# Optimization experiments

Hardware: AMD Instinct MI355X
Metric: run time of the kernel (lower is better)

## Reference

```python
import jax, jax.numpy as jnp
from jax import lax
import numpy as np

B, T = 128, 28
N = T - 1  # 27 recurrent steps


def conv(x, w, b, stride=1, pad=1):
    y = lax.conv_general_dilated(x, w, (stride, stride), [(pad, pad), (pad, pad)],
                                 dimension_numbers=('NCHW', 'OIHW', 'NCHW'))
    return y + b[None, :, None, None]


def convT(x, w, b, stride, pad, out_pad):
    # torch ConvTranspose2d: weight layout [in, out, k, k]
    k = w.shape[-1]
    wt = jnp.flip(w, (-2, -1)).transpose(1, 0, 2, 3)  # -> [out, in, k, k]
    lo, hi = k - 1 - pad, k - 1 - pad + out_pad
    y = lax.conv_general_dilated(x, wt, (1, 1), [(lo, hi), (lo, hi)],
                                 lhs_dilation=(stride, stride),
                                 dimension_numbers=('NCHW', 'OIHW', 'NCHW'))
    return y + b[None, :, None, None]


def setup_inputs():
    key = jax.random.key(0)
    ki = iter(jax.random.split(key, 48))
    def cw(o, i, k=3):
        return jax.random.normal(next(ki), (o, i, k, k), jnp.float32) / np.sqrt(i * k * k)
    def bias(o):
        return jax.random.normal(next(ki), (o,), jnp.float32) * 0.02
    H, I = 16 * 8 * 8, 48 * 8 * 8
    return {
        'x': jax.random.uniform(next(ki), (B, T, 3, 32, 32), jnp.float32),
        'eps': jax.random.normal(next(ki), (N, B, 64, 8, 8), jnp.float32),
        'psix1_w': cw(16, 3),  'psix1_b': bias(16),
        'psix2_w': cw(16, 16), 'psix2_b': bias(16),
        'psiz_w': cw(16, 64),  'psiz_b': bias(16),
        'enc1_w': cw(32, 32),  'enc1_b': bias(32),
        'enc2_w': cw(64, 32),  'enc2_b': bias(64),
        'encm_w': cw(64, 64),  'encm_b': bias(64),
        'encv_w': cw(64, 64),  'encv_b': bias(64),
        'pri_w': cw(32, 16),   'pri_b': bias(32),
        'prim_w': cw(64, 32),  'prim_b': bias(64),
        'priv_w': cw(64, 32),  'priv_b': bias(64),
        'dec1_w': jax.random.normal(next(ki), (32, 32, 3, 3), jnp.float32) / np.sqrt(32 * 9),
        'dec1_b': bias(32),
        'dec2_w': jax.random.normal(next(ki), (32, 3, 3, 3), jnp.float32) / np.sqrt(32 * 9),
        'dec2_b': bias(3),
        'gru_wi': jax.random.normal(next(ki), (3 * H, I), jnp.float32) / np.sqrt(I),
        'gru_wh': jax.random.normal(next(ki), (3 * H, H), jnp.float32) / np.sqrt(H),
        'gru_bi': bias(3 * H),
        'gru_bh': bias(3 * H),
    }


def _forward(x, eps, psix1_w, psix1_b, psix2_w, psix2_b, psiz_w, psiz_b,
             enc1_w, enc1_b, enc2_w, enc2_b, encm_w, encm_b, encv_w, encv_b,
             pri_w, pri_b, prim_w, prim_b, priv_w, priv_b,
             dec1_w, dec1_b, dec2_w, dec2_b, gru_wi, gru_wh, gru_bi, gru_bh):
    Bn = x.shape[0]
    Hf = 16 * 8 * 8
    n = x.shape[1] - 1

    def step(carry, inputs):
        h0, dec_prev, _, _, _, _ = carry
        frame, ep, idx = inputs
        cur = jnp.where(idx < 6, frame, dec_prev)
        px = jax.nn.relu(conv(cur, psix1_w, psix1_b, 2, 1))   # [B,16,16,16]
        px = jax.nn.relu(conv(px, psix2_w, psix2_b, 2, 1))    # [B,16,8,8]
        e = jnp.concatenate([px, h0], axis=1)                 # [B,32,8,8]
        e = jax.nn.relu(conv(e, enc1_w, enc1_b))
        e = jax.nn.relu(conv(e, enc2_w, enc2_b))              # [B,64,8,8]
        zm = conv(e, encm_w, encm_b)
        zlv = jax.nn.softplus(conv(e, encv_w, encv_b))
        p = jax.nn.relu(conv(h0, pri_w, pri_b))               # [B,32,8,8]
        pm = conv(p, prim_w, prim_b)
        plv = jax.nn.softplus(conv(p, priv_w, priv_b))
        z = zm + zlv * ep                                     # source's literal reparam (uses logvar, not std)
        zpsi = jax.nn.relu(conv(z, psiz_w, psiz_b))           # [B,16,8,8]
        d = jnp.concatenate([h0, zpsi], axis=1)               # [B,32,8,8]
        d = jax.nn.relu(convT(d, dec1_w, dec1_b, 2, 1, 0))    # 8 -> 15
        dec = jax.nn.sigmoid(convT(d, dec2_w, dec2_b, 2, 0, 1))  # 15 -> 32, [B,3,32,32]
        # GRUCell on flattened concat
        gi = jnp.concatenate([px, zpsi, h0], axis=1).reshape(Bn, -1)  # [B, 48*8*8]
        hf = h0.reshape(Bn, Hf)
        gih = gi @ gru_wi.T + gru_bi
        ghh = hf @ gru_wh.T + gru_bh
        ir, iz, inn = jnp.split(gih, 3, axis=1)
        hr, hz, hn = jnp.split(ghh, 3, axis=1)
        r = jax.nn.sigmoid(ir + hr)
        u = jax.nn.sigmoid(iz + hz)
        ng = jnp.tanh(inn + r * hn)
        hnew = ((1.0 - u) * ng + u * hf).reshape(Bn, 16, 8, 8)
        return (hnew, dec, zm, zlv, pm, plv), dec

    h0 = jnp.zeros((Bn, 16, 8, 8), jnp.float32)
    dec0 = jnp.zeros((Bn, 3, 32, 32), jnp.float32)
    s0 = jnp.zeros((Bn, 64, 8, 8), jnp.float32)
    frames = jnp.swapaxes(x[:, :n], 0, 1)  # [N,B,3,32,32]
    (_, _, zm, zlv, pm, plv), decs = lax.scan(
        step, (h0, dec0, s0, s0, s0, s0), (frames, eps, jnp.arange(n)))
    output = jnp.swapaxes(decs, 0, 1)  # [B,N,3,32,32]
    return output, zm, zlv, pm, plv


def reference(x, eps, psix1_w, psix1_b, psix2_w, psix2_b, psiz_w, psiz_b,
              enc1_w, enc1_b, enc2_w, enc2_b, encm_w, encm_b, encv_w, encv_b,
              pri_w, pri_b, prim_w, prim_b, priv_w, priv_b,
              dec1_w, dec1_b, dec2_w, dec2_b, gru_wi, gru_wh, gru_bi, gru_bh):
    return _forward(x, eps, psix1_w, psix1_b, psix2_w, psix2_b, psiz_w, psiz_b,
                    enc1_w, enc1_b, enc2_w, enc2_b, encm_w, encm_b, encv_w, encv_b,
                    pri_w, pri_b, prim_w, prim_b, priv_w, priv_b,
                    dec1_w, dec1_b, dec2_w, dec2_b, gru_wi, gru_wh, gru_bi, gru_bh)
```

## Files before the change

### kernel.cpp

```cpp
#include <hip/hip_runtime.h>

#define NSTEP 27

typedef _Float16 f16;
typedef __attribute__((ext_vector_type(8))) _Float16 f16x8;
typedef __attribute__((ext_vector_type(4))) float f32x4;

#define MFMA(a, b, c) __builtin_amdgcn_mfma_f32_16x16x32_f16(a, b, c, 0, 0, 0)

__device__ __forceinline__ float sigmoidf_(float x) { return 1.0f / (1.0f + expf(-x)); }
__device__ __forceinline__ float softplusf_(float x) { return x > 20.0f ? x : log1pf(expf(x)); }

constexpr long OFF_WI   = 0;
constexpr long OFF_WH   = OFF_WI   + 3072L * 3072;
constexpr long OFF_WPX1 = OFF_WH   + 3072L * 1024;
constexpr long OFF_WPX2 = OFF_WPX1 + 512;
constexpr long OFF_WE1  = OFF_WPX2 + 2560;
constexpr long OFF_WE2  = OFF_WE1  + 9216;
constexpr long OFF_WMV  = OFF_WE2  + 18432;
constexpr long OFF_WPZ  = OFF_WMV  + 73728;
constexpr long OFF_WPRI = OFF_WPZ  + 9216;
constexpr long OFF_WPMV = OFF_WPRI + 5120;
constexpr long OFF_WD1  = OFF_WPMV + 36864;
constexpr long OFF_GI   = OFF_WD1  + 9216;
constexpr long OFF_F16_END = OFF_GI + 128L * 3072;

struct Params {
  const float* frame; long fstride;
  const float* eps_t;
  const f16 *wpx1, *wpx2, *we1, *we2, *wmv, *wpz, *wd1, *wpri, *wpmv;
  const float *bpx1, *bpx2, *be1, *be2, *bm, *bv, *bpz, *bd1;
  const float *d2w, *d2b, *bpri, *bpm, *bpv, *gbi, *gbh;
  const float *gih0, *gih1, *ghh;
  float* hG; f16* gi;
  float *out_t, *zm, *zlv, *pm, *plv;
  int t, last;
};

__device__ __forceinline__ void scat8_lds(f16* __restrict__ A, int ldk, int pos, int ic, float val) {
  int py = pos >> 3, px = pos & 7;
  f16 v = (f16)val;
#pragma unroll
  for (int ky = 0; ky < 3; ++ky) {
    int oy = py + 1 - ky;
    if ((unsigned)oy >= 8u) continue;
#pragma unroll
    for (int kx = 0; kx < 3; ++kx) {
      int ox = px + 1 - kx;
      if ((unsigned)ox >= 8u) continue;
      A[(oy * 8 + ox) * ldk + ic * 9 + ky * 3 + kx] = v;
    }
  }
}

__device__ __forceinline__ void scatd1_lds(f16* __restrict__ Ad1, int pos, int ic, float val) {
  const int aof[4] = {0, 2560, 7168, 11776};
  const int Kp[4] = {40, 72, 72, 136};
  int py = pos >> 3, px = pos & 7;
  f16 v = (f16)val;
#pragma unroll
  for (int ky = 0; ky < 3; ++ky) {
    int y = 2 * py + ky - 1;
    if ((unsigned)y >= 15u) continue;
    int cy = y & 1;
    int nky = cy ? 2 : 1;
    int tiy = cy ? (ky >> 1) : 0;
#pragma unroll
    for (int kx = 0; kx < 3; ++kx) {
      int x = 2 * px + kx - 1;
      if ((unsigned)x >= 15u) continue;
      int cx = x & 1;
      int nkx = cx ? 2 : 1;
      int tix = cx ? (kx >> 1) : 0;
      int c = cy * 2 + cx;
      Ad1[aof[c] + ((y >> 1) * 8 + (x >> 1)) * Kp[c] + ic * (nky * nkx) + tiy * nkx + tix] = v;
    }
  }
}

__global__ __launch_bounds__(256) void k_wpack(const float* __restrict__ src, f16* __restrict__ dst,
                                               int N, int Ks, int Kd) {
  int tot = N * Kd, stride = gridDim.x * 256;
  for (int i = blockIdx.x * 256 + threadIdx.x; i < tot; i += stride) {
    int n = i / Kd, k = i - n * Kd;
    dst[i] = (k < Ks) ? (f16)src[n * Ks + k] : (f16)0.f;
  }
}

__global__ __launch_bounds__(256) void k_wd1(const float* __restrict__ src, f16* __restrict__ dst) {
  int i = blockIdx.x * 256 + threadIdx.x;
  if (i >= 9216) return;
  int c, base;
  if (i < 1024) { c = 0; base = 0; }
  else if (i < 3072) { c = 1; base = 1024; }
  else if (i < 5120) { c = 2; base = 3072; }
  else { c = 3; base = 5120; }
  const int Kc[4] = {32, 64, 64, 128};
  int j = i - base, K = Kc[c];
  int oc = j / K, k = j - oc * K;
  int cy = c >> 1, cx = c & 1;
  int nky = cy ? 2 : 1, nkx = cx ? 2 : 1, ntap = nky * nkx;
  int ic = k / ntap, tap = k - ic * ntap;
  int tiy = tap / nkx, tix = tap - tiy * nkx;
  int ky = (nky == 1) ? 1 : tiy * 2;
  int kx = (nkx == 1) ? 1 : tix * 2;
  dst[i] = (f16)src[((ic * 32 + oc) * 3 + ky) * 3 + kx];
}

__global__ __launch_bounds__(1024) void k_step(Params P) {
  __shared__ f16 lds[78336];
  f16* hbuf = lds;
  f16* B1 = lds + 1024;
  f16* B2 = lds + 38400;
  f16* B3 = lds + 57344;
  f16* A1 = B3;
  f16* frame = B3 + 10240;
  f16* A2 = B3 + 10240;

  int b = blockIdx.x, tid = threadIdx.x;
  int wv = tid >> 6, lane = tid & 63, lm = lane & 15, q = lane >> 4;
  f32x4 z4 = {};

  {
    int i = tid;
    float hn = 0.f;
    if (P.t) {
      long o = (long)b * 3072 + i;
      float ir  = P.gih0[o] + P.gih1[o] + P.gbi[i];
      float iz  = P.gih0[o + 1024] + P.gih1[o + 1024] + P.gbi[i + 1024];
      float in_ = P.gih0[o + 2048] + P.gih1[o + 2048] + P.gbi[i + 2048];
      float hr  = P.ghh[o] + P.gbh[i];
      float hz  = P.ghh[o + 1024] + P.gbh[i + 1024];
      float hnn = P.ghh[o + 2048] + P.gbh[i + 2048];
      float r = sigmoidf_(ir + hr), u = sigmoidf_(iz + hz);
      float ng = tanhf(in_ + r * hnn);
      hn = (1.f - u) * ng + u * P.hG[b * 1024 + i];
    }
    P.hG[b * 1024 + i] = hn;
    hbuf[i] = (f16)hn;
    P.gi[(long)b * 3072 + 2048 + i] = (f16)hn;
  }
  const float* fr = P.frame + (long)b * P.fstride;
  for (int i = tid; i < 3072; i += 1024) frame[i] = (f16)fr[i];
  __syncthreads();
  if (tid < 512) {
    int row = tid >> 1, half = tid & 1;
    int oy = row >> 4, ox = row & 15;
    f16* rp = A1 + row * 40;
    if (half == 0) {
#pragma unroll
      for (int ic = 0; ic < 2; ++ic)
#pragma unroll
        for (int ky = 0; ky < 3; ++ky) {
          int y = 2 * oy + ky - 1;
#pragma unroll
          for (int kx = 0; kx < 3; ++kx) {
            int x = 2 * ox + kx - 1;
            rp[ic * 9 + ky * 3 + kx] =
                ((unsigned)y < 32u && (unsigned)x < 32u) ? frame[ic * 1024 + y * 32 + x] : (f16)0;
          }
        }
    } else {
#pragma unroll
      for (int ky = 0; ky < 3; ++ky) {
        int y = 2 * oy + ky - 1;
#pragma unroll
        for (int kx = 0; kx < 3; ++kx) {
          int x = 2 * ox + kx - 1;
          rp[18 + ky * 3 + kx] =
              ((unsigned)y < 32u && (unsigned)x < 32u) ? frame[2048 + y * 32 + x] : (f16)0;
        }
      }
#pragma unroll
      for (int k = 27; k < 40; ++k) rp[k] = (f16)0;
    }
  } else {
    int4 zz = {0, 0, 0, 0};
    int t2 = tid - 512;
    for (int i = t2; i < 18944 / 8; i += 512) ((int4*)B2)[i] = zz;
    for (int i = t2; i < 37376 / 8; i += 512) ((int4*)B1)[i] = zz;
  }
  __syncthreads();
  {
    int4 zz = {0, 0, 0, 0};
    for (int i = tid; i < 10752 / 8; i += 1024) ((int4*)A2)[i] = zz;
  }
  __syncthreads();
  scat8_lds(B2, 296, tid & 63, 16 + (tid >> 6), (float)hbuf[tid]);
  {
    f16x8 bf = *(const f16x8*)(P.wpx1 + lm * 32 + q * 8);
    float bb = P.bpx1[lm];
    int mt = wv;
    f16x8 a = *(const f16x8*)(A1 + (mt * 16 + lm) * 40 + q * 8);
    f32x4 acc = MFMA(a, bf, z4);
#pragma unroll
    for (int r = 0; r < 4; ++r) {
      int m = mt * 16 + q * 4 + r;
      float val = fmaxf(acc[r] + bb, 0.f);
      int y = m >> 4, x = m & 15;
      f16 v = (f16)val;
#pragma unroll
      for (int ky = 0; ky < 3; ++ky) {
        int ty = y + 1 - ky;
        if (ty < 0 || (ty & 1)) continue;
        int oy = ty >> 1; if (oy >= 8) continue;
#pragma unroll
        for (int kx = 0; kx < 3; ++kx) {
          int tx = x + 1 - kx;
          if (tx < 0 || (tx & 1)) continue;
          int ox = tx >> 1; if (ox >= 8) continue;
          A2[(oy * 8 + ox) * 168 + lm * 9 + ky * 3 + kx] = v;
        }
      }
    }
  }
  __syncthreads();
  if (wv < 4) {
    f32x4 acc = {};
#pragma unroll
    for (int k = 0; k < 160; k += 32) {
      f16x8 a = *(const f16x8*)(A2 + (wv * 16 + lm) * 168 + k + q * 8);
      f16x8 bf = *(const f16x8*)(P.wpx2 + lm * 160 + k + q * 8);
      acc = MFMA(a, bf, acc);
    }
    float bb = P.bpx2[lm];
#pragma unroll
    for (int r = 0; r < 4; ++r) {
      int pos = wv * 16 + q * 4 + r;
      float val = fmaxf(acc[r] + bb, 0.f);
      P.gi[(long)b * 3072 + lm * 64 + pos] = (f16)val;
      scat8_lds(B2, 296, pos, lm, val);
    }
  }
  __syncthreads();
  {
    int nt = wv & 1, mt = (wv >> 1) & 3;
    f32x4 a0 = {};
    if (wv < 8) {
#pragma unroll
      for (int k = 0; k < 288; k += 32) {
        f16x8 bf = *(const f16x8*)(P.we1 + (nt * 16 + lm) * 288 + k + q * 8);
        f16x8 x0 = *(const f16x8*)(B2 + (mt * 16 + lm) * 296 + k + q * 8);
        a0 = MFMA(x0, bf, a0);
      }
    } else {
      int i0 = (wv - 8) * 128 + lane;
      scatd1_lds(B3, i0 & 63, i0 >> 6, (float)hbuf[i0]);
      int i1 = i0 + 64;
      scatd1_lds(B3, i1 & 63, i1 >> 6, (float)hbuf[i1]);
    }
    __syncthreads();
    if (wv < 8) {
      float bb = P.be1[nt * 16 + lm];
#pragma unroll
      for (int r = 0; r < 4; ++r)
        scat8_lds(B2, 296, mt * 16 + q * 4 + r, nt * 16 + lm, fmaxf(a0[r] + bb, 0.f));
    }
  }
  __syncthreads();
  {
    int nt = wv & 3, mh = wv >> 2;
    f32x4 acc = {};
#pragma unroll
    for (int k = 0; k < 288; k += 32) {
      f16x8 bf = *(const f16x8*)(P.we2 + (nt * 16 + lm) * 288 + k + q * 8);
      f16x8 a = *(const f16x8*)(B2 + ((mh)*16 + lm) * 296 + k + q * 8);
      acc = MFMA(a, bf, acc);
    }
    int ch = nt * 16 + lm;
    float bb = P.be2[ch];
#pragma unroll
    for (int r = 0; r < 4; ++r)
      scat8_lds(B1, 584, mh * 16 + q * 4 + r, ch, fmaxf(acc[r] + bb, 0.f));
  }
  __syncthreads();
  {
    f32x4 am = {}, av = {};
    int nq = wv & 3, mh = wv >> 2;
    int ch = nq * 16 + lm;
#pragma unroll
    for (int k = 0; k < 576; k += 32) {
      f16x8 bm = *(const f16x8*)(P.wmv + (long)ch * 576 + k + q * 8);
      f16x8 bv = *(const f16x8*)(P.wmv + (long)(64 + ch) * 576 + k + q * 8);
      f16x8 a = *(const f16x8*)(B1 + (mh * 16 + lm) * 584 + k + q * 8);
      am = MFMA(a, bm, am);
      av = MFMA(a, bv, av);
    }
    __syncthreads();
    float bbm = P.bm[ch], bbv = P.bv[ch];
#pragma unroll
    for (int r = 0; r < 4; ++r) {
      int pos = mh * 16 + q * 4 + r;
      float zmv = am[r] + bbm;
      float sp = softplusf_(av[r] + bbv);
      float zval = zmv + sp * P.eps_t[(long)b * 4096 + ch * 64 + pos];
      if (P.last) {
        P.zm[(long)b * 4096 + ch * 64 + pos] = zmv;
        P.zlv[(long)b * 4096 + ch * 64 + pos] = sp;
      }
      scat8_lds(B1, 584, pos, ch, zval);
    }
  }
  __syncthreads();
  if (wv < 4) {
    f32x4 acc = {};
#pragma unroll
    for (int k = 0; k < 576; k += 32) {
      f16x8 a = *(const f16x8*)(B1 + (wv * 16 + lm) * 584 + k + q * 8);
      f16x8 bf = *(const f16x8*)(P.wpz + (long)lm * 576 + k + q * 8);
      acc = MFMA(a, bf, acc);
    }
    float bb = P.bpz[lm];
#pragma unroll
    for (int r = 0; r < 4; ++r) {
      int pos = wv * 16 + q * 4 + r;
      float val = fmaxf(acc[r] + bb, 0.f);
      P.gi[(long)b * 3072 + 1024 + lm * 64 + pos] = (f16)val;
      scatd1_lds(B3, pos, 16 + lm, val);
    }
  }
  __syncthreads();
  {
    int nt = wv & 1, mt = (wv >> 1) & 3, cb = wv >> 3;
#pragma unroll
    for (int cc = 0; cc < 2; ++cc) {
      int c = cb + cc * 2;
      int cy = c >> 1, cx = c & 1;
      int Kc = 32 << (cy + cx);
      int Kp = Kc + 8;
      int aof = cy ? (cx ? 11776 : 7168) : (cx ? 2560 : 0);
      int bof = cy ? (cx ? 5120 : 3072) : (cx ? 1024 : 0);
      f32x4 acc = {};
      for (int k = 0; k < Kc; k += 32) {
        f16x8 a = *(const f16x8*)(B3 + aof + (mt * 16 + lm) * Kp + k + q * 8);
        f16x8 bf = *(const f16x8*)(P.wd1 + bof + (nt * 16 + lm) * Kc + k + q * 8);
        acc = MFMA(a, bf, acc);
      }
      int oc = nt * 16 + lm;
      float bb = P.bd1[oc];
#pragma unroll
      for (int r = 0; r < 4; ++r) {
        int m = mt * 16 + q * 4 + r;
        int y = 2 * (m >> 3) + cy, x = 2 * (m & 7) + cx;
        if (y < 15 && x < 15)
          B2[oc * 240 + y * 15 + x] = (f16)fmaxf(acc[r] + bb, 0.f);
      }
    }
  }
  __syncthreads();
  {
    int p = wv & 3, jh = wv >> 2;
    int cy2 = p >> 1, cx2 = p & 1;
    int lx = lane & 15, ly = lane >> 4;
    int x = 2 * lx + cx2;
    float acc0 = P.d2b[0], acc1 = P.d2b[1], acc2 = P.d2b[2];
    int nky = cy2 ? 1 : 2, nkx = cx2 ? 1 : 2;
    int py = jh * 4 + ly;
    for (int ic = 0; ic < 32; ++ic) {
      const f16* sp = B2 + ic * 240;
      const float* wic = P.d2w + ic * 27;
      for (int ty = 0; ty < nky; ++ty) {
        int ky = cy2 ? 1 : ty * 2;
        int iy = (2 * py + cy2 - ky) >> 1;
        bool yv = (unsigned)iy < 15u;
        for (int tx = 0; tx < nkx; ++tx) {
          int kx = cx2 ? 1 : tx * 2;
          int ix = (x - kx) >> 1;
          if (yv && (unsigned)ix < 15u) {
            float v = (float)sp[iy * 15 + ix];
            acc0 += v * wic[ky * 3 + kx];
            acc1 += v * wic[9 + ky * 3 + kx];
            acc2 += v * wic[18 + ky * 3 + kx];
          }
        }
      }
    }
    int y = 2 * py + cy2;
    P.out_t[(long)b * 82944 + 0 * 1024 + y * 32 + x] = sigmoidf_(acc0);
    P.out_t[(long)b * 82944 + 1 * 1024 + y * 32 + x] = sigmoidf_(acc1);
    P.out_t[(long)b * 82944 + 2 * 1024 + y * 32 + x] = sigmoidf_(acc2);
  }
  if (P.last) {
    if (tid < 64) {
      int py = tid >> 3, px = tid & 7;
      f16* rp = B3 + tid * 168;
      int k = 0;
      for (int ic = 0; ic < 16; ++ic)
        for (int ky = 0; ky < 3; ++ky) {
          int y = py + ky - 1;
          for (int kx = 0; kx < 3; ++kx, ++k) {
            int x = px + kx - 1;
            rp[k] = ((unsigned)y < 8u && (unsigned)x < 8u) ? hbuf[ic * 64 + y * 8 + x] : (f16)0;
          }
        }
      for (; k < 168; ++k) rp[k] = (f16)0;
    }
    {
      int4 zz = {0, 0, 0, 0};
      for (int i = tid; i < 18944 / 8; i += 1024) ((int4*)B1)[i] = zz;
    }
    __syncthreads();
    if (wv < 8) {
      int nt = wv & 1, mt = wv >> 1;
      f32x4 a0 = {};
#pragma unroll
      for (int k = 0; k < 160; k += 32) {
        f16x8 bf = *(const f16x8*)(P.wpri + (nt * 16 + lm) * 160 + k + q * 8);
        f16x8 x0 = *(const f16x8*)(B3 + (mt * 16 + lm) * 168 + k + q * 8);
        a0 = MFMA(x0, bf, a0);
      }
      float bb = P.bpri[nt * 16 + lm];
#pragma unroll
      for (int r = 0; r < 4; ++r)
        scat8_lds(B1, 296, mt * 16 + q * 4 + r, nt * 16 + lm, fmaxf(a0[r] + bb, 0.f));
    }
    __syncthreads();
    {
      f32x4 am = {}, av = {};
      int nq = wv & 3, mh = wv >> 2;
      int ch = nq * 16 + lm;
#pragma unroll
      for (int k = 0; k < 288; k += 32) {
        f16x8 bm = *(const f16x8*)(P.wpmv + (long)ch * 288 + k + q * 8);
        f16x8 bv = *(const f16x8*)(P.wpmv + (long)(64 + ch) * 288 + k + q * 8);
        f16x8 a = *(const f16x8*)(B1 + (mh * 16 + lm) * 296 + k + q * 8);
        am = MFMA(a, bm, am);
        av = MFMA(a, bv, av);
      }
      float bbm = P.bpm[ch], bbv = P.bpv[ch];
#pragma unroll
      for (int r = 0; r < 4; ++r) {
        int pos = mh * 16 + q * 4 + r;
        P.pm[(long)b * 4096 + ch * 64 + pos] = am[r] + bbm;
        P.plv[(long)b * 4096 + ch * 64 + pos] = softplusf_(av[r] + bbv);
      }
    }
  }
}

__global__ __launch_bounds__(128) void k_gru(const f16* __restrict__ gi,
                                             const f16* __restrict__ wi, const f16* __restrict__ wh,
                                             float* __restrict__ gih0, float* __restrict__ gih1,
                                             float* __restrict__ ghh) {
  int z = blockIdx.y;
  int wv = threadIdx.x >> 6, lane = threadIdx.x & 63, lm = lane & 15, q = lane >> 4;
  int gw = blockIdx.x * 2 + wv;
  int mg = gw & 1, ng = gw >> 1;
  const f16* A = (z == 2) ? gi + 2048 : gi;
  const f16* B = (z == 2) ? wh : wi;
  int K = (z == 2) ? 1024 : 1536;
  int k0 = (z == 1) ? 1536 : 0;
  long ldb = (z == 2) ? 1024 : 3072;
  float* out = (z == 0) ? gih0 : (z == 1) ? gih1 : ghh;
  int m0 = mg * 64, n0 = ng * 32;
  f32x4 acc[4][2] = {};
  const f16* Ap = A + (long)(m0 + lm) * 3072 + k0 + q * 8;
  const f16* Bp = B + (long)(n0 + lm) * ldb + k0 + q * 8;
#pragma unroll 2
  for (int k = 0; k < K; k += 32) {
    f16x8 b0 = *(const f16x8*)(Bp + k);
    f16x8 b1 = *(const f16x8*)(Bp + 16 * ldb + k);
#pragma unroll
    for (int i = 0; i < 4; ++i) {
      f16x8 a = *(const f16x8*)(Ap + (long)i * 16 * 3072 + k);
      acc[i][0] = MFMA(a, b0, acc[i][0]);
      acc[i][1] = MFMA(a, b1, acc[i][1]);
    }
  }
#pragma unroll
  for (int i = 0; i < 4; ++i)
#pragma unroll
    for (int j = 0; j < 2; ++j)
#pragma unroll
      for (int r = 0; r < 4; ++r)
        out[(long)(m0 + i * 16 + q * 4 + r) * 3072 + n0 + j * 16 + lm] = acc[i][j][r];
}

extern "C" void kernel_launch(void* const* d_in, const int* in_sizes, int n_in,
                              void* d_out, int out_size, void* d_ws, size_t ws_size,
                              hipStream_t stream) {
  const float* x       = (const float*)d_in[0];
  const float* eps     = (const float*)d_in[1];
  const float* psix1_w = (const float*)d_in[2];
  const float* psix1_b = (const float*)d_in[3];
  const float* psix2_w = (const float*)d_in[4];
  const float* psix2_b = (const float*)d_in[5];
  const float* psiz_w  = (const float*)d_in[6];
  const float* psiz_b  = (const float*)d_in[7];
  const float* enc1_w  = (const float*)d_in[8];
  const float* enc1_b  = (const float*)d_in[9];
  const float* enc2_w  = (const float*)d_in[10];
  const float* enc2_b  = (const float*)d_in[11];
  const float* encm_w  = (const float*)d_in[12];
  const float* encm_b  = (const float*)d_in[13];
  const float* encv_w  = (const float*)d_in[14];
  const float* encv_b  = (const float*)d_in[15];
  const float* pri_w   = (const float*)d_in[16];
  const float* pri_b   = (const float*)d_in[17];
  const float* prim_w  = (const float*)d_in[18];
  const float* prim_b  = (const float*)d_in[19];
  const float* priv_w  = (const float*)d_in[20];
  const float* priv_b  = (const float*)d_in[21];
  const float* dec1_w  = (const float*)d_in[22];
  const float* dec1_b  = (const float*)d_in[23];
  const float* dec2_w  = (const float*)d_in[24];
  const float* dec2_b  = (const float*)d_in[25];
  const float* gru_wi  = (const float*)d_in[26];
  const float* gru_wh  = (const float*)d_in[27];
  const float* gru_bi  = (const float*)d_in[28];
  const float* gru_bh  = (const float*)d_in[29];

  float* out = (float*)d_out;
  float* zm_out  = out + 10616832;
  float* zlv_out = zm_out + 524288;
  float* pm_out  = zlv_out + 524288;
  float* plv_out = pm_out + 524288;

  f16* ws16 = (f16*)d_ws;
  f16* wi_f  = ws16 + OFF_WI;
  f16* wh_f  = ws16 + OFF_WH;
  f16* w_px1 = ws16 + OFF_WPX1;
  f16* w_px2 = ws16 + OFF_WPX2;
  f16* w_e1  = ws16 + OFF_WE1;
  f16* w_e2  = ws16 + OFF_WE2;
  f16* w_mv  = ws16 + OFF_WMV;
  f16* w_pz  = ws16 + OFF_WPZ;
  f16* w_pri = ws16 + OFF_WPRI;
  f16* w_pmv = ws16 + OFF_WPMV;
  f16* w_d1  = ws16 + OFF_WD1;
  f16* gi    = ws16 + OFF_GI;
  float* fws = (float*)(ws16 + OFF_F16_END);
  float* gih0 = fws;
  float* gih1 = gih0 + 393216;
  float* ghh  = gih1 + 393216;
  float* hG   = ghh + 393216;

  k_wpack<<<2048, 256, 0, stream>>>(gru_wi, wi_f, 3072, 3072, 3072);
  k_wpack<<<1024, 256, 0, stream>>>(gru_wh, wh_f, 3072, 1024, 1024);
  k_wpack<<<2, 256, 0, stream>>>(psix1_w, w_px1, 16, 27, 32);
  k_wpack<<<10, 256, 0, stream>>>(psix2_w, w_px2, 16, 144, 160);
  k_wpack<<<36, 256, 0, stream>>>(enc1_w, w_e1, 32, 288, 288);
  k_wpack<<<72, 256, 0, stream>>>(enc2_w, w_e2, 64, 288, 288);
  k_wpack<<<144, 256, 0, stream>>>(encm_w, w_mv, 64, 576, 576);
  k_wpack<<<144, 256, 0, stream>>>(encv_w, w_mv + 64L * 576, 64, 576, 576);
  k_wpack<<<36, 256, 0, stream>>>(psiz_w, w_pz, 16, 576, 576);
  k_wpack<<<20, 256, 0, stream>>>(pri_w, w_pri, 32, 144, 160);
  k_wpack<<<72, 256, 0, stream>>>(prim_w, w_pmv, 64, 288, 288);
  k_wpack<<<72, 256, 0, stream>>>(priv_w, w_pmv + 64L * 288, 64, 288, 288);
  k_wd1<<<36, 256, 0, stream>>>(dec1_w, w_d1);

  for (int t = 0; t < NSTEP; ++t) {
    Params P;
    P.frame = (t < 6) ? x + (long)t * 3072 : out + (long)(t - 1) * 3072;
    P.fstride = (t < 6) ? 86016 : 82944;
    P.eps_t = eps + (long)t * 524288;
    P.wpx1 = w_px1; P.wpx2 = w_px2; P.we1 = w_e1; P.we2 = w_e2;
    P.wmv = w_mv; P.wpz = w_pz; P.wd1 = w_d1; P.wpri = w_pri; P.wpmv = w_pmv;
    P.bpx1 = psix1_b; P.bpx2 = psix2_b; P.be1 = enc1_b; P.be2 = enc2_b;
    P.bm = encm_b; P.bv = encv_b; P.bpz = psiz_b; P.bd1 = dec1_b;
    P.d2w = dec2_w; P.d2b = dec2_b; P.bpri = pri_b; P.bpm = prim_b; P.bpv = priv_b;
    P.gbi = gru_bi; P.gbh = gru_bh;
    P.gih0 = gih0; P.gih1 = gih1; P.ghh = ghh;
    P.hG = hG; P.gi = gi;
    P.out_t = out + (long)t * 3072;
    P.zm = zm_out; P.zlv = zlv_out; P.pm = pm_out; P.plv = plv_out;
    P.t = t; P.last = (t == NSTEP - 1);
    k_step<<<128, 1024, 0, stream>>>(P);
    if (t < NSTEP - 1)
      k_gru<<<dim3(96, 3), 128, 0, stream>>>(gi, wi_f, wh_f, gih0, gih1, ghh);
  }
}
```

Measured before the change: 2.710 ms.

## Fuse GRU GEMM into step kernel as spin-waiting blocks overlapping the decoder

The separate k_gru launch is removed, and its GEMM work now runs in 128 extra blocks of k_step. These extra blocks spin on global atomic counters that the 128 batch blocks increment once the hidden state and the psiz features are written to gi. The GRU projections for the next step can then overlap with the decoder and prior stages of the current step, and one kernel launch per step goes away. The eps load for the reparameterisation is also hoisted ahead of the encoder MFMA loop. The cost is reliance on all 256 blocks being co-resident, since spin-waiting can deadlock otherwise, plus added atomic and fence traffic.

```diff
diff --git a/kernel.cpp b/kernel.cpp
--- a/kernel.cpp
+++ b/kernel.cpp
@@ -29,10 +29,12 @@
   const float* frame; long fstride;
   const float* eps_t;
   const f16 *wpx1, *wpx2, *we1, *we2, *wmv, *wpz, *wd1, *wpri, *wpmv;
+  const f16 *wiG, *whG;
   const float *bpx1, *bpx2, *be1, *be2, *bm, *bv, *bpz, *bd1;
   const float *d2w, *d2b, *bpri, *bpm, *bpv, *gbi, *gbh;
   const float *gih0, *gih1, *ghh;
   float* hG; f16* gi;
+  int* ctr;
   float *out_t, *zm, *zlv, *pm, *plv;
   int t, last;
 };
@@ -109,6 +111,54 @@
 
 __global__ __launch_bounds__(1024) void k_step(Params P) {
   __shared__ f16 lds[78336];
+  int tid = threadIdx.x;
+  int wv = tid >> 6, lane = tid & 63, lm = lane & 15, q = lane >> 4;
+
+  if (blockIdx.x >= 128) {
+    if (P.t >= NSTEP - 1) return;
+    int gb = blockIdx.x - 128;
+    int cnt = (gb < 64) ? 5 : 4;
+    int base = (gb < 64) ? gb * 5 : 320 + (gb - 64) * 4;
+    if (wv >= cnt) return;
+    int tau = base + wv;
+    int z = tau / 192, gw = tau % 192;
+    int mg = gw & 1, ng = gw >> 1;
+    int* cp = P.ctr + ((z == 2) ? P.t : 32 + P.t);
+    if (lane == 0) {
+      while (atomicAdd(cp, 0) < 128) __builtin_amdgcn_s_sleep(32);
+    }
+    __threadfence();
+    const f16* A = (z == 2) ? P.gi + 2048 : P.gi;
+    const f16* B = (z == 2) ? P.whG : P.wiG;
+    int K = (z == 2) ? 1024 : 1536;
+    int k0 = (z == 1) ? 1536 : 0;
+    long ldb = (z == 2) ? 1024 : 3072;
+    float* outp = (z == 0) ? (float*)P.gih0 : (z == 1) ? (float*)P.gih1 : (float*)P.ghh;
+    int m0 = mg * 64, n0 = ng * 32;
+    f32x4 acc[4][2] = {};
+    const f16* Ap = A + (long)(m0 + lm) * 3072 + k0 + q * 8;
+    const f16* Bp = B + (long)(n0 + lm) * ldb + k0 + q * 8;
+#pragma unroll 2
+    for (int k = 0; k < K; k += 32) {
+      f16x8 b0 = *(const f16x8*)(Bp + k);
+      f16x8 b1 = *(const f16x8*)(Bp + 16 * ldb + k);
+#pragma unroll
+      for (int i = 0; i < 4; ++i) {
+        f16x8 a = *(const f16x8*)(Ap + (long)i * 16 * 3072 + k);
+        acc[i][0] = MFMA(a, b0, acc[i][0]);
+        acc[i][1] = MFMA(a, b1, acc[i][1]);
+      }
+    }
+#pragma unroll
+    for (int i = 0; i < 4; ++i)
+#pragma unroll
+      for (int j = 0; j < 2; ++j)
+#pragma unroll
+        for (int r = 0; r < 4; ++r)
+          outp[(long)(m0 + i * 16 + q * 4 + r) * 3072 + n0 + j * 16 + lm] = acc[i][j][r];
+    return;
+  }
+
   f16* hbuf = lds;
   f16* B1 = lds + 1024;
   f16* B2 = lds + 38400;
@@ -117,8 +167,7 @@
   f16* frame = B3 + 10240;
   f16* A2 = B3 + 10240;
 
-  int b = blockIdx.x, tid = threadIdx.x;
-  int wv = tid >> 6, lane = tid & 63, lm = lane & 15, q = lane >> 4;
+  int b = blockIdx.x;
   f32x4 z4 = {};
 
   {
@@ -143,6 +192,7 @@
   const float* fr = P.frame + (long)b * P.fstride;
   for (int i = tid; i < 3072; i += 1024) frame[i] = (f16)fr[i];
   __syncthreads();
+  if (tid == 0) { __threadfence(); atomicAdd(P.ctr + P.t, 1); }
   if (tid < 512) {
     int row = tid >> 1, half = tid & 1;
     int oy = row >> 4, ox = row & 15;
@@ -278,6 +328,8 @@
     f32x4 am = {}, av = {};
     int nq = wv & 3, mh = wv >> 2;
     int ch = nq * 16 + lm;
+    const float4 ev = *(const float4*)(P.eps_t + (long)b * 4096 + ch * 64 + mh * 16 + q * 4);
+    float evr[4] = {ev.x, ev.y, ev.z, ev.w};
 #pragma unroll
     for (int k = 0; k < 576; k += 32) {
       f16x8 bm = *(const f16x8*)(P.wmv + (long)ch * 576 + k + q * 8);
@@ -293,7 +345,7 @@
       int pos = mh * 16 + q * 4 + r;
       float zmv = am[r] + bbm;
       float sp = softplusf_(av[r] + bbv);
-      float zval = zmv + sp * P.eps_t[(long)b * 4096 + ch * 64 + pos];
+      float zval = zmv + sp * evr[r];
       if (P.last) {
         P.zm[(long)b * 4096 + ch * 64 + pos] = zmv;
         P.zlv[(long)b * 4096 + ch * 64 + pos] = sp;
@@ -320,6 +372,7 @@
     }
   }
   __syncthreads();
+  if (tid == 0) { __threadfence(); atomicAdd(P.ctr + 32 + P.t, 1); }
   {
     int nt = wv & 1, mt = (wv >> 1) & 3, cb = wv >> 3;
 #pragma unroll
@@ -436,44 +489,6 @@
       }
     }
   }
-}
-
-__global__ __launch_bounds__(128) void k_gru(const f16* __restrict__ gi,
-                                             const f16* __restrict__ wi, const f16* __restrict__ wh,
-                                             float* __restrict__ gih0, float* __restrict__ gih1,
-                                             float* __restrict__ ghh) {
-  int z = blockIdx.y;
-  int wv = threadIdx.x >> 6, lane = threadIdx.x & 63, lm = lane & 15, q = lane >> 4;
-  int gw = blockIdx.x * 2 + wv;
-  int mg = gw & 1, ng = gw >> 1;
-  const f16* A = (z == 2) ? gi + 2048 : gi;
-  const f16* B = (z == 2) ? wh : wi;
-  int K = (z == 2) ? 1024 : 1536;
-  int k0 = (z == 1) ? 1536 : 0;
-  long ldb = (z == 2) ? 1024 : 3072;
-  float* out = (z == 0) ? gih0 : (z == 1) ? gih1 : ghh;
-  int m0 = mg * 64, n0 = ng * 32;
-  f32x4 acc[4][2] = {};
-  const f16* Ap = A + (long)(m0 + lm) * 3072 + k0 + q * 8;
-  const f16* Bp = B + (long)(n0 + lm) * ldb + k0 + q * 8;
-#pragma unroll 2
-  for (int k = 0; k < K; k += 32) {
-    f16x8 b0 = *(const f16x8*)(Bp + k);
-    f16x8 b1 = *(const f16x8*)(Bp + 16 * ldb + k);
-#pragma unroll
-    for (int i = 0; i < 4; ++i) {
-      f16x8 a = *(const f16x8*)(Ap + (long)i * 16 * 3072 + k);
-      acc[i][0] = MFMA(a, b0, acc[i][0]);
-      acc[i][1] = MFMA(a, b1, acc[i][1]);
-    }
-  }
-#pragma unroll
-  for (int i = 0; i < 4; ++i)
-#pragma unroll
-    for (int j = 0; j < 2; ++j)
-#pragma unroll
-      for (int r = 0; r < 4; ++r)
-        out[(long)(m0 + i * 16 + q * 4 + r) * 3072 + n0 + j * 16 + lm] = acc[i][j][r];
 }
 
 extern "C" void kernel_launch(void* const* d_in, const int* in_sizes, int n_in,
@@ -534,6 +549,9 @@
   float* gih1 = gih0 + 393216;
   float* ghh  = gih1 + 393216;
   float* hG   = ghh + 393216;
+  int*   ctr  = (int*)(hG + 131072);
+
+  hipMemsetAsync(ctr, 0, 64 * sizeof(int), stream);
 
   k_wpack<<<2048, 256, 0, stream>>>(gru_wi, wi_f, 3072, 3072, 3072);
   k_wpack<<<1024, 256, 0, stream>>>(gru_wh, wh_f, 3072, 1024, 1024);
@@ -556,17 +574,17 @@
     P.eps_t = eps + (long)t * 524288;
     P.wpx1 = w_px1; P.wpx2 = w_px2; P.we1 = w_e1; P.we2 = w_e2;
     P.wmv = w_mv; P.wpz = w_pz; P.wd1 = w_d1; P.wpri = w_pri; P.wpmv = w_pmv;
+    P.wiG = wi_f; P.whG = wh_f;
     P.bpx1 = psix1_b; P.bpx2 = psix2_b; P.be1 = enc1_b; P.be2 = enc2_b;
     P.bm = encm_b; P.bv = encv_b; P.bpz = psiz_b; P.bd1 = dec1_b;
     P.d2w = dec2_w; P.d2b = dec2_b; P.bpri = pri_b; P.bpm = prim_b; P.bpv = priv_b;
     P.gbi = gru_bi; P.gbh = gru_bh;
     P.gih0 = gih0; P.gih1 = gih1; P.ghh = ghh;
     P.hG = hG; P.gi = gi;
+    P.ctr = ctr;
     P.out_t = out + (long)t * 3072;
     P.zm = zm_out; P.zlv = zlv_out; P.pm = pm_out; P.plv = plv_out;
     P.t = t; P.last = (t == NSTEP - 1);
-    k_step<<<128, 1024, 0, stream>>>(P);
-    if (t < NSTEP - 1)
-      k_gru<<<dim3(96, 3), 128, 0, stream>>>(gi, wi_f, wh_f, gih0, gih1, ghh);
+    k_step<<<256, 1024, 0, stream>>>(P);
   }
 }
```

After: 3.190 ms. 17.7% more time.
